# Kernel tuning notes

Measured on AMD Instinct MI355X. Metric: run time of the kernel, lower is better.

Reference implementation:

```python
import jax, jax.numpy as jnp
import numpy as np

# Module config (init_kwargs): shape_data=(5,32,32), pow=1, diff_only=False
N_T, N_Y, N_X = 5, 32, 32
N = N_Y * N_X          # nb_nodes = 1024
N_B = 2                # batch
DX = DY = DT = 1.0


def softplus_b(x, beta):
    # torch F.softplus(x, beta) = (1/beta) * log(1 + exp(beta*x))
    return jax.nn.softplus(beta * x) / beta


def build_A(kappa, m, H):
    """Dense finite-difference SPDE operator A = kappa^2 I + m.grad - div(H grad).
    kappa: (N,), m: (2,N), H: (2,2,N). Returns (N,N).
    (DiffOperator source is not in the provided snippet; this is the standard
    4dvarnet SPDE 9-point stencil discretization with dx=dy=1.)"""
    idx = jnp.arange(N)
    xx = idx % N_X
    yy = idx // N_X
    H11, H22 = H[0, 0], H[1, 1]
    H12 = 0.5 * (H[0, 1] + H[1, 0])
    m1, m2 = m[0], m[1]
    center = kappa ** 2 + 2.0 * H11 + 2.0 * H22
    A = jnp.zeros((N, N), dtype=kappa.dtype).at[idx, idx].set(center)
    stencil = [
        ( 1,  0, -H11 + 0.5 * m1),
        (-1,  0, -H11 - 0.5 * m1),
        ( 0,  1, -H22 + 0.5 * m2),
        ( 0, -1, -H22 - 0.5 * m2),
        ( 1,  1, -0.5 * H12),
        (-1, -1, -0.5 * H12),
        ( 1, -1,  0.5 * H12),
        (-1,  1,  0.5 * H12),
    ]
    for dxo, dyo, c in stencil:
        nx_, ny_ = xx + dxo, yy + dyo
        valid = (nx_ >= 0) & (nx_ < N_X) & (ny_ >= 0) & (ny_ < N_Y)
        nbr = jnp.clip(ny_, 0, N_Y - 1) * N_X + jnp.clip(nx_, 0, N_X - 1)
        A = A.at[idx, nbr].add(jnp.where(valid, c, 0.0))
    return A


def decode_params(params):
    """Faithful decode_param_CNN.forward (including its raw-reshape axis mixing)."""
    nb = params.shape[0]
    kappa = softplus_b(params[:, :N_T], 10.0)
    kappa = kappa.reshape(nb, 1, N, N_T)                     # raw reshape as in torch
    m = jnp.stack([params[:, N_T:2 * N_T], params[:, 2 * N_T:3 * N_T]], axis=1)
    m = m.reshape(nb, 2, N, N_T)                             # raw reshape as in torch
    gamma = softplus_b(params[:, 3 * N_T:4 * N_T], 10.0)
    gamma = gamma.transpose(0, 2, 3, 1).reshape(nb, N * N_T)  # (y,x,t) order
    vx = params[:, 4 * N_T:5 * N_T].transpose(0, 2, 3, 1).reshape(nb, N * N_T)
    vy = params[:, 5 * N_T:6 * N_T].transpose(0, 2, 3, 1).reshape(nb, N * N_T)
    vxy = jnp.stack([vx, vy], axis=2)                        # (b, K, 2)
    # H[b,i,j,k] = gamma[b,k]*delta_ij + v_i[b,k]*v_j[b,k]
    H = (jnp.eye(2, dtype=params.dtype)[None, :, :, None] * gamma[:, None, None, :]
         + jnp.einsum('bki,bkj->bijk', vxy, vxy))
    H = H.reshape(nb, 2, 2, N, N_T)
    return kappa, m, H


def reference(params):
    """Prior_SPDE.forward(decode_param_CNN(params), square_root=False) -> dense Q.
    Note: in create_Q (diff_only=False) tau is overwritten with ones and
    QR/Q0 are reassigned to Id / B0^T B0, so tau channels are dead code."""
    kappa, m, H = decode_params(params)
    # operators built for time indices k+1, k=0..n_t-2
    kap_t = jnp.moveaxis(kappa[:, 0, :, 1:], -1, 1).reshape(N_B * (N_T - 1), N)
    m_t = jnp.moveaxis(m[:, :, :, 1:], -1, 1).reshape(N_B * (N_T - 1), 2, N)
    H_t = jnp.moveaxis(H[:, :, :, :, 1:], -1, 1).reshape(N_B * (N_T - 1), 2, 2, N)
    A = jax.vmap(build_A)(kap_t, m_t, H_t).reshape(N_B, N_T - 1, N, N)
    I = jnp.eye(N, dtype=params.dtype)
    invM = A * DT + I                      # Id + dt*B, B = A (pow=1)
    M2 = jnp.matmul(invM, invM)            # inv_M[i]^2
    B0 = A[:, 0]
    Q = jnp.zeros((N_B, N_T * N, N_T * N), dtype=params.dtype)
    s = lambda i: slice(i * N, (i + 1) * N)
    # row 0: [B0^T B0 + I, -inv_M[0], 0...]
    Q = Q.at[:, s(0), s(0)].set(jnp.einsum('bki,bkj->bij', B0, B0) + I)
    Q = Q.at[:, s(0), s(1)].set(-invM[:, 0])
    # rows 1..n_t-2: [..., -inv_M[i-1], inv_M[i-1]^2 + I, -inv_M[i], ...]
    for i in range(1, N_T - 1):
        Q = Q.at[:, s(i), s(i - 1)].set(-invM[:, i - 1])
        Q = Q.at[:, s(i), s(i)].set(M2[:, i - 1] + I)
        Q = Q.at[:, s(i), s(i + 1)].set(-invM[:, i])
    # last row: [..., -inv_M[n_t-2], inv_M[n_t-2]^2]
    Q = Q.at[:, s(N_T - 1), s(N_T - 2)].set(-invM[:, N_T - 2])
    Q = Q.at[:, s(N_T - 1), s(N_T - 1)].set(M2[:, N_T - 2])
    Q = 0.5 * (Q + jnp.swapaxes(Q, 1, 2)) + 0.05 * jnp.eye(N_T * N, dtype=params.dtype)
    return Q


def setup_inputs() -> dict:
    key = jax.random.key(0)
    params = jax.random.normal(key, (N_B, 7 * N_T, N_Y, N_X), dtype=jnp.float32)
    return {"params": params}
```

## Files before the change

kernel.cpp:

```cpp
#include <hip/hip_runtime.h>


__device__ __forceinline__ float softplus10(float x) {
  float z = 10.f * x;
  return (fmaxf(z, 0.f) + log1pf(expf(-fabsf(z)))) * 0.1f;
}

__global__ __launch_bounds__(256) void decode_kernel(
    const float* __restrict__ P0, float* __restrict__ Ac) {
  int gid = blockIdx.x * 256 + threadIdx.x;
  if (gid >= 8 * 1024) return;
  int i = gid >> 10;
  int p = gid & 1023;
  int b = i >> 2;
  int t = (i & 3) + 1;
  const float* P = P0 + b * 35 * 1024;

  int qq = p * 5 + t;
  int c  = qq >> 10;
  int r  = qq & 1023;
  float kap = softplus10(P[(0 + c) * 1024 + r]);
  float m1  = P[(5 + c) * 1024 + r];
  float m2  = P[(10 + c) * 1024 + r];

  float g  = softplus10(P[(15 + t) * 1024 + p]);
  float vx = P[(20 + t) * 1024 + p];
  float vy = P[(25 + t) * 1024 + p];

  float H11 = g + vx * vx;
  float H22 = g + vy * vy;
  float H12 = vx * vy;

  float co[9];
  co[4] = kap * kap + 2.f * H11 + 2.f * H22;
  co[5] = -H11 + 0.5f * m1;
  co[3] = -H11 - 0.5f * m1;
  co[7] = -H22 + 0.5f * m2;
  co[1] = -H22 - 0.5f * m2;
  co[8] = -0.5f * H12;
  co[0] = -0.5f * H12;
  co[2] =  0.5f * H12;
  co[6] =  0.5f * H12;

  int px = p & 31, py = p >> 5;
  #pragma unroll
  for (int o = 0; o < 9; o++) {
    const int dx = o % 3 - 1, dy = o / 3 - 1;
    int nx = px + dx, ny = py + dy;
    bool valid = (nx >= 0) & (nx < 32) & (ny >= 0) & (ny < 32);
    Ac[(i * 1024 + p) * 9 + o] = (o == 4) ? co[4] : (valid ? co[o] : 0.f);
  }
}

__device__ __forceinline__ float m2e(const float* __restrict__ Ac, int i, int p, int q) {
  int px = p & 31, py = p >> 5, qx = q & 31, qy = q >> 5;
  float s = 0.f;
  #pragma unroll
  for (int o = 0; o < 9; o++) {
    const int dx = o % 3 - 1, dy = o / 3 - 1;
    int kx = px + dx, ky = py + dy;
    if (kx < 0 || kx > 31 || ky < 0 || ky > 31) continue;
    int k = ky * 32 + kx;
    float a = Ac[(i * 1024 + p) * 9 + o] + (o == 4 ? 1.f : 0.f);
    int ddx = qx - kx, ddy = qy - ky;
    if (ddx < -1 || ddx > 1 || ddy < -1 || ddy > 1) continue;
    float bb = Ac[(i * 1024 + k) * 9 + (ddy + 1) * 3 + (ddx + 1)]
             + (k == q ? 1.f : 0.f);
    s += a * bb;
  }
  return s;
}

__device__ __forceinline__ float btb(const float* __restrict__ Ac, int i0, int p, int q) {
  int px = p & 31, py = p >> 5, qx = q & 31, qy = q >> 5;
  float s = 0.f;
  #pragma unroll
  for (int o = 0; o < 9; o++) {
    const int dx = o % 3 - 1, dy = o / 3 - 1;
    int kx = px + dx, ky = py + dy;
    if (kx < 0 || kx > 31 || ky < 0 || ky > 31) continue;
    int k = ky * 32 + kx;
    float bkp = Ac[(i0 * 1024 + k) * 9 + (8 - o)];
    int ddx = qx - kx, ddy = qy - ky;
    if (ddx < -1 || ddx > 1 || ddy < -1 || ddy > 1) continue;
    float bkq = Ac[(i0 * 1024 + k) * 9 + (ddy + 1) * 3 + (ddx + 1)];
    s += bkp * bkq;
  }
  return s;
}

__global__ __launch_bounds__(256) void fill_kernel(
    const float* __restrict__ Ac, float4* __restrict__ out) {
  const int cb  = blockIdx.x;
  const int row = blockIdx.y;
  const int b   = blockIdx.z;
  const int tx  = threadIdx.x;
  const int rb  = row >> 10;
  const int p   = row & 1023;
  const int d   = cb - rb;
  const int oidx = b * 6553600 + row * 1280 + cb * 256 + tx;

  float4 v = make_float4(0.f, 0.f, 0.f, 0.f);
  if (d >= -1 && d <= 1) {
    const int q0 = tx * 4;
    const int px = p & 31, py = p >> 5;
    float rr[4] = {0.f, 0.f, 0.f, 0.f};
    if (d != 0) {
      const int i = b * 4 + (d > 0 ? rb : cb);
      #pragma unroll
      for (int j = 0; j < 4; j++) {
        int q = q0 + j;
        int dx = (q & 31) - px, dy = (q >> 5) - py;
        if (dx >= -1 && dx <= 1 && dy >= -1 && dy <= 1) {
          int o = (dy + 1) * 3 + (dx + 1);
          float s = Ac[(i * 1024 + p) * 9 + o]
                  + Ac[(i * 1024 + q) * 9 + (8 - o)];
          if (p == q) s += 2.f;
          rr[j] = -0.5f * s;
        }
      }
    } else if (rb == 0) {
      const int i0 = b * 4;
      #pragma unroll
      for (int j = 0; j < 4; j++) {
        int q = q0 + j;
        int dx = (q & 31) - px, dy = (q >> 5) - py;
        if (dx >= -2 && dx <= 2 && dy >= -2 && dy <= 2) {
          rr[j] = btb(Ac, i0, p, q) + (p == q ? 1.05f : 0.f);
        }
      }
    } else {
      const int i = b * 4 + rb - 1;
      const float diagAdd = (rb <= 3 ? 1.05f : 0.05f);
      #pragma unroll
      for (int j = 0; j < 4; j++) {
        int q = q0 + j;
        int dx = (q & 31) - px, dy = (q >> 5) - py;
        if (dx >= -2 && dx <= 2 && dy >= -2 && dy <= 2) {
          float m2s = 0.5f * (m2e(Ac, i, p, q) + m2e(Ac, i, q, p));
          rr[j] = m2s + (p == q ? diagAdd : 0.f);
        }
      }
    }
    v = make_float4(rr[0], rr[1], rr[2], rr[3]);
  }
  out[oidx] = v;
}

extern "C" void kernel_launch(void* const* d_in, const int* in_sizes, int n_in,
                              void* d_out, int out_size, void* d_ws, size_t ws_size,
                              hipStream_t stream) {
  const float* params = (const float*)d_in[0];
  float* Ac = (float*)d_ws;
  float4* out = (float4*)d_out;

  decode_kernel<<<32, 256, 0, stream>>>(params, Ac);
  dim3 grid(5, 5120, 2);
  fill_kernel<<<grid, 256, 0, stream>>>(Ac, out);
}
```

Measured before the change: 211.8 us.

## Precompute compact stencil coefficients for off-diagonal and diagonal blocks

Adds two small kernels that precompute, per node, the 9-point off-diagonal block values and the 25-point diagonal block values (B0^T B0 and symmetrized M^2) into workspace. The large fill kernel then only gathers from these compact tables instead of evaluating stencil products per output element. This removes redundant arithmetic and scattered loads from the store-bound fill pass, at the cost of two extra kernel launches and extra workspace traffic.

```diff
diff --git a/kernel.cpp b/kernel.cpp
--- a/kernel.cpp
+++ b/kernel.cpp
@@ -1,5 +1,9 @@
 #include <hip/hip_runtime.h>
 
+
+#define AC_OFF   0
+#define OFFD_OFF 73728
+#define DIAG_OFF 147456
 
 __device__ __forceinline__ float softplus10(float x) {
   float z = 10.f * x;
@@ -52,6 +56,30 @@
   }
 }
 
+__global__ __launch_bounds__(256) void offdiag_kernel(float* __restrict__ ws) {
+  const float* Ac = ws + AC_OFF;
+  float* offd = ws + OFFD_OFF;
+  int gid = blockIdx.x * 256 + threadIdx.x;
+  if (gid >= 8 * 1024) return;
+  int i = gid >> 10, p = gid & 1023;
+  int px = p & 31, py = p >> 5;
+  #pragma unroll
+  for (int o = 0; o < 9; o++) {
+    const int dx = o % 3 - 1, dy = o / 3 - 1;
+    float v = 0.f;
+    if (o == 4) {
+      v = -(Ac[(i * 1024 + p) * 9 + 4] + 1.f);
+    } else {
+      int nx = px + dx, ny = py + dy;
+      if (nx >= 0 && nx < 32 && ny >= 0 && ny < 32) {
+        int q = ny * 32 + nx;
+        v = -0.5f * (Ac[(i * 1024 + p) * 9 + o] + Ac[(i * 1024 + q) * 9 + (8 - o)]);
+      }
+    }
+    offd[(i * 1024 + p) * 9 + o] = v;
+  }
+}
+
 __device__ __forceinline__ float m2e(const float* __restrict__ Ac, int i, int p, int q) {
   int px = p & 31, py = p >> 5, qx = q & 31, qy = q >> 5;
   float s = 0.f;
@@ -64,8 +92,7 @@
     float a = Ac[(i * 1024 + p) * 9 + o] + (o == 4 ? 1.f : 0.f);
     int ddx = qx - kx, ddy = qy - ky;
     if (ddx < -1 || ddx > 1 || ddy < -1 || ddy > 1) continue;
-    float bb = Ac[(i * 1024 + k) * 9 + (ddy + 1) * 3 + (ddx + 1)]
-             + (k == q ? 1.f : 0.f);
+    float bb = Ac[(i * 1024 + k) * 9 + (ddy + 1) * 3 + (ddx + 1)] + (k == q ? 1.f : 0.f);
     s += a * bb;
   }
   return s;
@@ -89,8 +116,35 @@
   return s;
 }
 
+__global__ __launch_bounds__(256) void diagblk_kernel(float* __restrict__ ws) {
+  const float* Ac = ws + AC_OFF;
+  float* diag = ws + DIAG_OFF;
+  int gid = blockIdx.x * 256 + threadIdx.x;
+  if (gid >= 10 * 1024) return;
+  int j = gid >> 10, p = gid & 1023;
+  int b = j / 5, rb = j % 5;
+  int px = p & 31, py = p >> 5;
+  #pragma unroll
+  for (int w = 0; w < 25; w++) {
+    const int dx = w % 5 - 2, dy = w / 5 - 2;
+    int nx = px + dx, ny = py + dy;
+    float v = 0.f;
+    if (nx >= 0 && nx < 32 && ny >= 0 && ny < 32) {
+      int q = ny * 32 + nx;
+      if (rb == 0) {
+        v = btb(Ac, b * 4, p, q) + (p == q ? 1.05f : 0.f);
+      } else {
+        int i = b * 4 + rb - 1;
+        float diagAdd = (rb <= 3 ? 1.05f : 0.05f);
+        v = 0.5f * (m2e(Ac, i, p, q) + m2e(Ac, i, q, p)) + (p == q ? diagAdd : 0.f);
+      }
+    }
+    diag[(j * 1024 + p) * 25 + w] = v;
+  }
+}
+
 __global__ __launch_bounds__(256) void fill_kernel(
-    const float* __restrict__ Ac, float4* __restrict__ out) {
+    const float* __restrict__ ws, float4* __restrict__ out) {
   const int cb  = blockIdx.x;
   const int row = blockIdx.y;
   const int b   = blockIdx.z;
@@ -98,47 +152,34 @@
   const int rb  = row >> 10;
   const int p   = row & 1023;
   const int d   = cb - rb;
-  const int oidx = b * 6553600 + row * 1280 + cb * 256 + tx;
+  const long oidx = (long)b * 6553600 + (long)row * 1280 + cb * 256 + tx;
 
   float4 v = make_float4(0.f, 0.f, 0.f, 0.f);
   if (d >= -1 && d <= 1) {
-    const int q0 = tx * 4;
-    const int px = p & 31, py = p >> 5;
+    const int q0  = tx * 4;
+    const int qy  = q0 >> 5;
+    const int qx0 = q0 & 31;
+    const int px  = p & 31, py = p >> 5;
+    const int dy  = qy - py;
     float rr[4] = {0.f, 0.f, 0.f, 0.f};
     if (d != 0) {
-      const int i = b * 4 + (d > 0 ? rb : cb);
-      #pragma unroll
-      for (int j = 0; j < 4; j++) {
-        int q = q0 + j;
-        int dx = (q & 31) - px, dy = (q >> 5) - py;
-        if (dx >= -1 && dx <= 1 && dy >= -1 && dy <= 1) {
-          int o = (dy + 1) * 3 + (dx + 1);
-          float s = Ac[(i * 1024 + p) * 9 + o]
-                  + Ac[(i * 1024 + q) * 9 + (8 - o)];
-          if (p == q) s += 2.f;
-          rr[j] = -0.5f * s;
+      if (dy >= -1 && dy <= 1) {
+        const int i = b * 4 + (d > 0 ? rb : cb);
+        const float* t = ws + OFFD_OFF + ((i * 1024 + p) * 9 + (dy + 1) * 3 + 1) - px;
+        #pragma unroll
+        for (int jj = 0; jj < 4; jj++) {
+          int dx = qx0 + jj - px;
+          if (dx >= -1 && dx <= 1) rr[jj] = t[qx0 + jj];
         }
       }
-    } else if (rb == 0) {
-      const int i0 = b * 4;
-      #pragma unroll
-      for (int j = 0; j < 4; j++) {
-        int q = q0 + j;
-        int dx = (q & 31) - px, dy = (q >> 5) - py;
-        if (dx >= -2 && dx <= 2 && dy >= -2 && dy <= 2) {
-          rr[j] = btb(Ac, i0, p, q) + (p == q ? 1.05f : 0.f);
-        }
-      }
     } else {
-      const int i = b * 4 + rb - 1;
-      const float diagAdd = (rb <= 3 ? 1.05f : 0.05f);
-      #pragma unroll
-      for (int j = 0; j < 4; j++) {
-        int q = q0 + j;
-        int dx = (q & 31) - px, dy = (q >> 5) - py;
-        if (dx >= -2 && dx <= 2 && dy >= -2 && dy <= 2) {
-          float m2s = 0.5f * (m2e(Ac, i, p, q) + m2e(Ac, i, q, p));
-          rr[j] = m2s + (p == q ? diagAdd : 0.f);
+      if (dy >= -2 && dy <= 2) {
+        const int j = b * 5 + rb;
+        const float* t = ws + DIAG_OFF + ((j * 1024 + p) * 25 + (dy + 2) * 5 + 2) - px;
+        #pragma unroll
+        for (int jj = 0; jj < 4; jj++) {
+          int dx = qx0 + jj - px;
+          if (dx >= -2 && dx <= 2) rr[jj] = t[qx0 + jj];
         }
       }
     }
@@ -151,10 +192,12 @@
                               void* d_out, int out_size, void* d_ws, size_t ws_size,
                               hipStream_t stream) {
   const float* params = (const float*)d_in[0];
-  float* Ac = (float*)d_ws;
+  float* ws = (float*)d_ws;
   float4* out = (float4*)d_out;
 
-  decode_kernel<<<32, 256, 0, stream>>>(params, Ac);
+  decode_kernel<<<32, 256, 0, stream>>>(params, ws + AC_OFF);
+  offdiag_kernel<<<32, 256, 0, stream>>>(ws);
+  diagblk_kernel<<<40, 256, 0, stream>>>(ws);
   dim3 grid(5, 5120, 2);
-  fill_kernel<<<grid, 256, 0, stream>>>(Ac, out);
-}
+  fill_kernel<<<grid, 256, 0, stream>>>(ws, out);
+}
```

Measured after the change: 225.3 us. 6.4% more time.
